# Kernel tuning notes

Hardware: AMD Instinct MI355X
Metric: run time of the kernel (lower is better)

Reference implementation:

```python
import jax, jax.numpy as jnp
import numpy as np

S, V, E, H = 4096, 10000, 128, 256
NE, TK, NH, HD, FF, NL = 4, 2, 4, 64, 2048, 2
EPS = 1e-5
SCALE = 1.0 / np.sqrt(HD).astype(np.float32)


def setup_inputs() -> dict:
    key = jax.random.key(0)
    ks = iter(jax.random.split(key, 64))
    n = lambda shape: jax.random.normal(next(ks), shape, jnp.float32) * 0.02
    inp = {"x": jax.random.randint(next(ks), (S,), 0, V)}
    inp["emb"] = n((V, E))
    for i, din in enumerate([E, H, H]):
        inp[f"moe{i}_gw"] = n((NE, din))
        inp[f"moe{i}_gb"] = jnp.zeros((NE,), jnp.float32)
        inp[f"moe{i}_ew"] = n((NE, H, din))
        inp[f"moe{i}_eb"] = jnp.zeros((NE, H), jnp.float32)
    inp["attn_in_w"] = n((NL, 3 * H, H)); inp["attn_in_b"] = jnp.zeros((NL, 3 * H), jnp.float32)
    inp["attn_out_w"] = n((NL, H, H));    inp["attn_out_b"] = jnp.zeros((NL, H), jnp.float32)
    inp["ln1_g"] = jnp.ones((NL, H), jnp.float32); inp["ln1_b"] = jnp.zeros((NL, H), jnp.float32)
    inp["ln2_g"] = jnp.ones((NL, H), jnp.float32); inp["ln2_b"] = jnp.zeros((NL, H), jnp.float32)
    inp["ff1_w"] = n((NL, FF, H)); inp["ff1_b"] = jnp.zeros((NL, FF), jnp.float32)
    inp["ff2_w"] = n((NL, H, FF)); inp["ff2_b"] = jnp.zeros((NL, H), jnp.float32)
    inp["fc_w"] = n((H, H)); inp["fc_b"] = jnp.zeros((H,), jnp.float32)
    inp["out_w"] = n((V, H)); inp["out_b"] = jnp.zeros((V,), jnp.float32)
    return inp


def _ln(x, g, b):
    m = x.mean(-1, keepdims=True)
    v = ((x - m) ** 2).mean(-1, keepdims=True)
    return (x - m) * jax.lax.rsqrt(v + EPS) * g + b


def _moe(x, gw, gb, ew, eb):
    # x: [S, din]. Faithful quirk: experts are the top-k of TOKEN 0's gates,
    # applied to every token, weighted by each token's own top-k gate scores.
    scores = jax.nn.softmax(x @ gw.T + gb, axis=-1)            # [S, NE]
    vals, idx = jax.lax.top_k(scores, TK)                      # [S, TK]
    sel = idx[0]                                               # [TK]
    outs = jnp.einsum('si,khi->skh', x, ew[sel]) + eb[sel][None]  # [S, TK, H]
    return (outs * vals[:, :, None]).sum(axis=1)               # [S, H]


def reference(x, emb,
              moe0_gw, moe0_gb, moe0_ew, moe0_eb,
              moe1_gw, moe1_gb, moe1_ew, moe1_eb,
              moe2_gw, moe2_gb, moe2_ew, moe2_eb,
              attn_in_w, attn_in_b, attn_out_w, attn_out_b,
              ln1_g, ln1_b, ln2_g, ln2_b,
              ff1_w, ff1_b, ff2_w, ff2_b,
              fc_w, fc_b, out_w, out_b):
    h = emb[x]                                                 # [S, E]
    for gw, gb, ew, eb in [(moe0_gw, moe0_gb, moe0_ew, moe0_eb),
                           (moe1_gw, moe1_gb, moe1_ew, moe1_eb),
                           (moe2_gw, moe2_gb, moe2_ew, moe2_eb)]:
        h = _moe(h, gw, gb, ew, eb)                            # [S, H]
    for l in range(NL):  # post-norm TransformerEncoderLayer (relu, no dropout at eval)
        qkv = h @ attn_in_w[l].T + attn_in_b[l]                # [S, 3H]
        q, k, v = [t.reshape(S, NH, HD) for t in jnp.split(qkv, 3, axis=-1)]
        att = jax.nn.softmax(jnp.einsum('shd,thd->hst', q, k) * SCALE, axis=-1)
        a = jnp.einsum('hst,thd->shd', att, v).reshape(S, H)
        h = _ln(h + a @ attn_out_w[l].T + attn_out_b[l], ln1_g[l], ln1_b[l])
        ffh = jax.nn.relu(h @ ff1_w[l].T + ff1_b[l]) @ ff2_w[l].T + ff2_b[l]
        h = _ln(h + ffh, ln2_g[l], ln2_b[l])
    h = h @ fc_w.T + fc_b                                      # [S, H]
    logits = h @ out_w.T + out_b                               # [S, V]
    return jax.nn.log_softmax(logits, axis=-1)
```

## Files before the change

kernel.cpp:

```cpp
#include <hip/hip_runtime.h>
#include <math.h>

#define S_ 4096
#define V_ 10000
#define E_ 128
#define H_ 256
#define NE_ 4
#define NH_ 4
#define HD_ 64
#define FF_ 2048
#define NL_ 2
#define EPS_ 1e-5f
#define SCALE_ 0.125f
#define SPLITS_ 4
#define PSTRIDE_ 160

typedef __attribute__((ext_vector_type(8))) short bf16x8;
typedef __attribute__((ext_vector_type(4))) float f32x4;

static __device__ __forceinline__ short f2bf(float f) {
  unsigned u = __builtin_bit_cast(unsigned, f);
  unsigned r = (u + 0x7fffu + ((u >> 16) & 1u)) >> 16;
  return (short)r;
}
static __device__ __forceinline__ float bf2f(short s) {
  unsigned u = ((unsigned)(unsigned short)s) << 16;
  return __builtin_bit_cast(float, u);
}

struct CvtArgs {
  const float* src[9];
  short* dst[9];
  int pfx[10];
};
__global__ __launch_bounds__(256) void k_cvt(CvtArgs a, const int* __restrict__ x,
                                             const float* __restrict__ emb,
                                             short* __restrict__ h) {
  int b = blockIdx.x;
  if (b >= a.pfx[9]) {
    int i8 = (b - a.pfx[9]) * 2048 + threadIdx.x * 8;
    int s = i8 >> 7, e = i8 & 127;
    const float* sp = &emb[(size_t)x[s] * E_ + e];
    float4 v0 = *(const float4*)sp;
    float4 v1 = *(const float4*)(sp + 4);
    short4 o0, o1;
    o0.x = f2bf(v0.x); o0.y = f2bf(v0.y); o0.z = f2bf(v0.z); o0.w = f2bf(v0.w);
    o1.x = f2bf(v1.x); o1.y = f2bf(v1.y); o1.z = f2bf(v1.z); o1.w = f2bf(v1.w);
    *(short4*)&h[i8] = o0;
    *(short4*)&h[i8 + 4] = o1;
    return;
  }
  int s = 0;
  while (b >= a.pfx[s + 1]) ++s;
  size_t base = (size_t)(b - a.pfx[s]) * 2048 + threadIdx.x * 8;
  const float* sp = a.src[s] + base;
  short* dp = a.dst[s] + base;
  float4 v0 = *(const float4*)sp;
  float4 v1 = *(const float4*)(sp + 4);
  short4 o0, o1;
  o0.x = f2bf(v0.x); o0.y = f2bf(v0.y); o0.z = f2bf(v0.z); o0.w = f2bf(v0.w);
  o1.x = f2bf(v1.x); o1.y = f2bf(v1.y); o1.z = f2bf(v1.z); o1.w = f2bf(v1.w);
  *(short4*)dp = o0;
  *(short4*)(dp + 4) = o1;
}

__global__ __launch_bounds__(256) void k_gates(const short* __restrict__ X, int din,
                                               const float* __restrict__ gw,
                                               const float* __restrict__ gb,
                                               float* __restrict__ vals,
                                               int* __restrict__ sel) {
  int wave = threadIdx.x >> 6, lane = threadIdx.x & 63;
  int s = blockIdx.x * 4 + wave;
  const short* xs = X + (size_t)s * din;
  float a0 = 0.f, a1 = 0.f, a2 = 0.f, a3 = 0.f;
  for (int i = lane; i < din; i += 64) {
    float xv = bf2f(xs[i]);
    a0 += xv * gw[0 * din + i];
    a1 += xv * gw[1 * din + i];
    a2 += xv * gw[2 * din + i];
    a3 += xv * gw[3 * din + i];
  }
#pragma unroll
  for (int off = 32; off > 0; off >>= 1) {
    a0 += __shfl_xor(a0, off, 64);
    a1 += __shfl_xor(a1, off, 64);
    a2 += __shfl_xor(a2, off, 64);
    a3 += __shfl_xor(a3, off, 64);
  }
  if (lane == 0) {
    float sc[4] = {a0 + gb[0], a1 + gb[1], a2 + gb[2], a3 + gb[3]};
    float mx = fmaxf(fmaxf(sc[0], sc[1]), fmaxf(sc[2], sc[3]));
    float sum = 0.f;
#pragma unroll
    for (int e = 0; e < 4; ++e) { sc[e] = expf(sc[e] - mx); sum += sc[e]; }
    float inv = 1.0f / sum;
#pragma unroll
    for (int e = 0; e < 4; ++e) sc[e] *= inv;
    int i0 = 0; float v0 = sc[0];
#pragma unroll
    for (int e = 1; e < 4; ++e) if (sc[e] > v0) { v0 = sc[e]; i0 = e; }
    float v1 = -1.0f; int i1 = 0;
#pragma unroll
    for (int e = 0; e < 4; ++e) if (e != i0 && sc[e] > v1) { v1 = sc[e]; i1 = e; }
    vals[2 * s + 0] = v0;
    vals[2 * s + 1] = v1;
    if (s == 0) { sel[0] = i0; sel[1] = i1; }
  }
}

template <int ACT>
__global__ __launch_bounds__(256) void k_gemm64(const short* __restrict__ A,
                                                const short* __restrict__ W,
                                                const float* __restrict__ bias,
                                                short* __restrict__ C,
                                                int M, int N, int K) {
  __shared__ short As[64][40];
  __shared__ short Bs[64][40];
  int bm = blockIdx.y * 64, bn = blockIdx.x * 64;
  int tid = threadIdx.x, lane = tid & 63, wv = tid >> 6;
  int quad = lane >> 4, m16 = lane & 15;
  int wr = (wv >> 1) * 32, wc = (wv & 1) * 32;
  int srow = tid >> 2, sc = (tid & 3) * 8;
  const short* Ar = A + (size_t)(bm + srow) * K + sc;
  const short* Wr = W + (size_t)(bn + srow) * K + sc;
  f32x4 acc[2][2];
#pragma unroll
  for (int m = 0; m < 2; ++m)
#pragma unroll
    for (int n = 0; n < 2; ++n) acc[m][n] = (f32x4){0.f, 0.f, 0.f, 0.f};
  for (int k0 = 0; k0 < K; k0 += 32) {
    *(bf16x8*)&As[srow][sc] = *(const bf16x8*)&Ar[k0];
    *(bf16x8*)&Bs[srow][sc] = *(const bf16x8*)&Wr[k0];
    __syncthreads();
    bf16x8 af[2], bf[2];
#pragma unroll
    for (int m = 0; m < 2; ++m) af[m] = *(const bf16x8*)&As[wr + m * 16 + m16][quad * 8];
#pragma unroll
    for (int n = 0; n < 2; ++n) bf[n] = *(const bf16x8*)&Bs[wc + n * 16 + m16][quad * 8];
#pragma unroll
    for (int m = 0; m < 2; ++m)
#pragma unroll
      for (int n = 0; n < 2; ++n)
        acc[m][n] = __builtin_amdgcn_mfma_f32_16x16x32_bf16(af[m], bf[n], acc[m][n], 0, 0, 0);
    __syncthreads();
  }
#pragma unroll
  for (int n = 0; n < 2; ++n) {
    int col = bn + wc + n * 16 + m16;
    float b = bias[col];
#pragma unroll
    for (int m = 0; m < 2; ++m) {
      int row0 = bm + wr + m * 16 + quad * 4;
#pragma unroll
      for (int r = 0; r < 4; ++r) {
        float v = acc[m][n][r] + b;
        if (ACT) v = fmaxf(v, 0.f);
        C[(size_t)(row0 + r) * N + col] = f2bf(v);
      }
    }
  }
}

template <int ACT>
__global__ __launch_bounds__(256) void k_gemm32(const short* __restrict__ A,
                                                const short* __restrict__ W,
                                                const float* __restrict__ bias,
                                                short* __restrict__ C,
                                                int M, int N, int K) {
  __shared__ short As[32][40];
  __shared__ short Bs[64][40];
  int bm = blockIdx.y * 32, bn = blockIdx.x * 64;
  int tid = threadIdx.x, lane = tid & 63, wv = tid >> 6;
  int quad = lane >> 4, m16 = lane & 15;
  int wr = (wv >> 1) * 16, wc = (wv & 1) * 32;
  int srow = tid >> 2, sc = (tid & 3) * 8;
  const short* Ar = A + (size_t)(bm + (srow & 31)) * K + sc;
  const short* Wr = W + (size_t)(bn + srow) * K + sc;
  f32x4 acc[2];
  acc[0] = (f32x4){0.f, 0.f, 0.f, 0.f};
  acc[1] = (f32x4){0.f, 0.f, 0.f, 0.f};
  for (int k0 = 0; k0 < K; k0 += 32) {
    if (tid < 128) *(bf16x8*)&As[srow][sc] = *(const bf16x8*)&Ar[k0];
    *(bf16x8*)&Bs[srow][sc] = *(const bf16x8*)&Wr[k0];
    __syncthreads();
    bf16x8 af = *(const bf16x8*)&As[wr + m16][quad * 8];
    bf16x8 bf0 = *(const bf16x8*)&Bs[wc + m16][quad * 8];
    bf16x8 bf1 = *(const bf16x8*)&Bs[wc + 16 + m16][quad * 8];
    acc[0] = __builtin_amdgcn_mfma_f32_16x16x32_bf16(af, bf0, acc[0], 0, 0, 0);
    acc[1] = __builtin_amdgcn_mfma_f32_16x16x32_bf16(af, bf1, acc[1], 0, 0, 0);
    __syncthreads();
  }
#pragma unroll
  for (int n = 0; n < 2; ++n) {
    int col = bn + wc + n * 16 + m16;
    float b = bias[col];
    int row0 = bm + wr + quad * 4;
#pragma unroll
    for (int r = 0; r < 4; ++r) {
      float v = acc[n][r] + b;
      if (ACT) v = fmaxf(v, 0.f);
      C[(size_t)(row0 + r) * N + col] = f2bf(v);
    }
  }
}

__global__ __launch_bounds__(256) void k_proj(const float* __restrict__ Opart,
                                              const float* __restrict__ Lpart,
                                              const short* __restrict__ W,
                                              const float* __restrict__ bias,
                                              short* __restrict__ C) {
  __shared__ short As[32][40];
  __shared__ short Bs[64][40];
  int bm = blockIdx.y * 32, bn = blockIdx.x * 64;
  int tid = threadIdx.x, lane = tid & 63, wv = tid >> 6;
  int quad = lane >> 4, m16 = lane & 15;
  int wr = (wv >> 1) * 16, wc = (wv & 1) * 32;
  int srow = tid >> 2, sc = (tid & 3) * 8;
  int rowA = bm + (srow & 31);
  const short* Wr = W + (size_t)(bn + srow) * H_ + sc;
  float invden[NH_];
  if (tid < 128) {
#pragma unroll
    for (int hh = 0; hh < NH_; ++hh) {
      float dsum = 0.f;
#pragma unroll
      for (int sp = 0; sp < SPLITS_; ++sp)
        dsum += Lpart[(size_t)(sp * NH_ + hh) * S_ + rowA];
      invden[hh] = 1.0f / dsum;
    }
  }
  f32x4 acc[2];
  acc[0] = (f32x4){0.f, 0.f, 0.f, 0.f};
  acc[1] = (f32x4){0.f, 0.f, 0.f, 0.f};
#pragma unroll
  for (int k0 = 0; k0 < H_; k0 += 32) {
    if (tid < 128) {
      const int head = k0 >> 6;
      int dd = (k0 & 63) + sc;
      float n0 = 0.f, n1 = 0.f, n2 = 0.f, n3 = 0.f, n4 = 0.f, n5 = 0.f, n6 = 0.f, n7 = 0.f;
#pragma unroll
      for (int sp = 0; sp < SPLITS_; ++sp) {
        const float* op = &Opart[((size_t)(sp * NH_ + head) * S_ + rowA) * 64 + dd];
        float4 u0 = *(const float4*)op;
        float4 u1 = *(const float4*)(op + 4);
        n0 += u0.x; n1 += u0.y; n2 += u0.z; n3 += u0.w;
        n4 += u1.x; n5 += u1.y; n6 += u1.z; n7 += u1.w;
      }
      float iv = invden[head];
      union { short s[8]; bf16x8 v; } o;
      o.s[0] = f2bf(n0 * iv); o.s[1] = f2bf(n1 * iv);
      o.s[2] = f2bf(n2 * iv); o.s[3] = f2bf(n3 * iv);
      o.s[4] = f2bf(n4 * iv); o.s[5] = f2bf(n5 * iv);
      o.s[6] = f2bf(n6 * iv); o.s[7] = f2bf(n7 * iv);
      *(bf16x8*)&As[srow][sc] = o.v;
    }
    *(bf16x8*)&Bs[srow][sc] = *(const bf16x8*)&Wr[k0];
    __syncthreads();
    bf16x8 af = *(const bf16x8*)&As[wr + m16][quad * 8];
    bf16x8 bf0 = *(const bf16x8*)&Bs[wc + m16][quad * 8];
    bf16x8 bf1 = *(const bf16x8*)&Bs[wc + 16 + m16][quad * 8];
    acc[0] = __builtin_amdgcn_mfma_f32_16x16x32_bf16(af, bf0, acc[0], 0, 0, 0);
    acc[1] = __builtin_amdgcn_mfma_f32_16x16x32_bf16(af, bf1, acc[1], 0, 0, 0);
    __syncthreads();
  }
#pragma unroll
  for (int n = 0; n < 2; ++n) {
    int col = bn + wc + n * 16 + m16;
    float b = bias[col];
    int row0 = bm + wr + quad * 4;
#pragma unroll
    for (int r = 0; r < 4; ++r) {
      float v = acc[n][r] + b;
      C[(size_t)(row0 + r) * H_ + col] = f2bf(v);
    }
  }
}

__global__ __launch_bounds__(256) void k_ff2(const short* __restrict__ A,
                                             const short* __restrict__ W,
                                             const float* __restrict__ bias,
                                             short* __restrict__ C) {
  __shared__ short As[32][72];
  __shared__ short Bs[64][72];
  int bm = blockIdx.y * 32, bn = blockIdx.x * 64;
  int tid = threadIdx.x, lane = tid & 63, wv = tid >> 6;
  int quad = lane >> 4, m16 = lane & 15;
  int wr = (wv >> 1) * 16, wc = (wv & 1) * 32;
  int arow = tid >> 3, ac = (tid & 7) * 8;
  int brow = tid >> 2, bc = (tid & 3) * 16;
  const short* Ar = A + (size_t)(bm + arow) * FF_ + ac;
  const short* Wr = W + (size_t)(bn + brow) * FF_ + bc;
  f32x4 acc[2];
  acc[0] = (f32x4){0.f, 0.f, 0.f, 0.f};
  acc[1] = (f32x4){0.f, 0.f, 0.f, 0.f};
  for (int k0 = 0; k0 < FF_; k0 += 64) {
    *(bf16x8*)&As[arow][ac] = *(const bf16x8*)&Ar[k0];
    *(bf16x8*)&Bs[brow][bc] = *(const bf16x8*)&Wr[k0];
    *(bf16x8*)&Bs[brow][bc + 8] = *(const bf16x8*)&Wr[k0 + 8];
    __syncthreads();
    bf16x8 af0 = *(const bf16x8*)&As[wr + m16][quad * 8];
    bf16x8 af1 = *(const bf16x8*)&As[wr + m16][32 + quad * 8];
    bf16x8 b00 = *(const bf16x8*)&Bs[wc + m16][quad * 8];
    bf16x8 b01 = *(const bf16x8*)&Bs[wc + m16][32 + quad * 8];
    bf16x8 b10 = *(const bf16x8*)&Bs[wc + 16 + m16][quad * 8];
    bf16x8 b11 = *(const bf16x8*)&Bs[wc + 16 + m16][32 + quad * 8];
    acc[0] = __builtin_amdgcn_mfma_f32_16x16x32_bf16(af0, b00, acc[0], 0, 0, 0);
    acc[0] = __builtin_amdgcn_mfma_f32_16x16x32_bf16(af1, b01, acc[0], 0, 0, 0);
    acc[1] = __builtin_amdgcn_mfma_f32_16x16x32_bf16(af0, b10, acc[1], 0, 0, 0);
    acc[1] = __builtin_amdgcn_mfma_f32_16x16x32_bf16(af1, b11, acc[1], 0, 0, 0);
    __syncthreads();
  }
#pragma unroll
  for (int n = 0; n < 2; ++n) {
    int col = bn + wc + n * 16 + m16;
    float b = bias[col];
    int row0 = bm + wr + quad * 4;
#pragma unroll
    for (int r = 0; r < 4; ++r) {
      float v = acc[n][r] + b;
      C[(size_t)(row0 + r) * H_ + col] = f2bf(v);
    }
  }
}

__global__ __launch_bounds__(256) void k_moe(const short* __restrict__ A,
                                             const short* __restrict__ EW,
                                             const float* __restrict__ EB,
                                             const float* __restrict__ vals,
                                             const int* __restrict__ sel,
                                             short* __restrict__ C,
                                             int N, int K) {
  __shared__ short As[32][40];
  __shared__ short B0s[64][40];
  __shared__ short B1s[64][40];
  int e0 = sel[0], e1 = sel[1];
  const short* W0 = EW + (size_t)e0 * N * K;
  const short* W1 = EW + (size_t)e1 * N * K;
  const float* b0 = EB + (size_t)e0 * N;
  const float* b1 = EB + (size_t)e1 * N;
  int bm = blockIdx.y * 32, bn = blockIdx.x * 64;
  int tid = threadIdx.x, lane = tid & 63, wv = tid >> 6;
  int quad = lane >> 4, m16 = lane & 15;
  int wr = (wv >> 1) * 16, wc = (wv & 1) * 32;
  int srow = tid >> 2, sc = (tid & 3) * 8;
  const short* Ar = A + (size_t)(bm + (srow & 31)) * K + sc;
  const short* W0r = W0 + (size_t)(bn + srow) * K + sc;
  const short* W1r = W1 + (size_t)(bn + srow) * K + sc;
  f32x4 a0[2], a1[2];
  a0[0] = a0[1] = (f32x4){0.f, 0.f, 0.f, 0.f};
  a1[0] = a1[1] = (f32x4){0.f, 0.f, 0.f, 0.f};
  for (int k0 = 0; k0 < K; k0 += 32) {
    if (tid < 128) *(bf16x8*)&As[srow][sc] = *(const bf16x8*)&Ar[k0];
    *(bf16x8*)&B0s[srow][sc] = *(const bf16x8*)&W0r[k0];
    *(bf16x8*)&B1s[srow][sc] = *(const bf16x8*)&W1r[k0];
    __syncthreads();
    bf16x8 af = *(const bf16x8*)&As[wr + m16][quad * 8];
#pragma unroll
    for (int n = 0; n < 2; ++n) {
      bf16x8 bf0 = *(const bf16x8*)&B0s[wc + n * 16 + m16][quad * 8];
      bf16x8 bf1 = *(const bf16x8*)&B1s[wc + n * 16 + m16][quad * 8];
      a0[n] = __builtin_amdgcn_mfma_f32_16x16x32_bf16(af, bf0, a0[n], 0, 0, 0);
      a1[n] = __builtin_amdgcn_mfma_f32_16x16x32_bf16(af, bf1, a1[n], 0, 0, 0);
    }
    __syncthreads();
  }
#pragma unroll
  for (int n = 0; n < 2; ++n) {
    int col = bn + wc + n * 16 + m16;
    float bb0 = b0[col], bb1 = b1[col];
    int row0 = bm + wr + quad * 4;
#pragma unroll
    for (int r = 0; r < 4; ++r) {
      int row = row0 + r;
      float v = vals[2 * row] * (a0[n][r] + bb0) + vals[2 * row + 1] * (a1[n][r] + bb1);
      C[(size_t)row * N + col] = f2bf(v);
    }
  }
}

template <int ACT>
__global__ __launch_bounds__(256) void k_gemm128(const short* __restrict__ A,
                                                 const short* __restrict__ W,
                                                 const float* __restrict__ bias,
                                                 short* __restrict__ C,
                                                 int M, int N, int K) {
  __shared__ short As[128][40];
  __shared__ short Bs[128][40];
  int bm = blockIdx.y * 128, bn = blockIdx.x * 128;
  int tid = threadIdx.x, lane = tid & 63, wv = tid >> 6;
  int quad = lane >> 4, m16 = lane & 15;
  int wr = (wv >> 1) * 64, wc = (wv & 1) * 64;
  int srow = tid >> 1, sc = (tid & 1) * 16;
  const short* Ar = A + (size_t)(bm + srow) * K + sc;
  const short* Wr = W + (size_t)(bn + srow) * K + sc;
  f32x4 acc[4][4];
#pragma unroll
  for (int m = 0; m < 4; ++m)
#pragma unroll
    for (int n = 0; n < 4; ++n) acc[m][n] = (f32x4){0.f, 0.f, 0.f, 0.f};
  for (int k0 = 0; k0 < K; k0 += 32) {
    *(bf16x8*)&As[srow][sc] = *(const bf16x8*)&Ar[k0];
    *(bf16x8*)&As[srow][sc + 8] = *(const bf16x8*)&Ar[k0 + 8];
    *(bf16x8*)&Bs[srow][sc] = *(const bf16x8*)&Wr[k0];
    *(bf16x8*)&Bs[srow][sc + 8] = *(const bf16x8*)&Wr[k0 + 8];
    __syncthreads();
    bf16x8 af[4], bf[4];
#pragma unroll
    for (int m = 0; m < 4; ++m) af[m] = *(const bf16x8*)&As[wr + m * 16 + m16][quad * 8];
#pragma unroll
    for (int n = 0; n < 4; ++n) bf[n] = *(const bf16x8*)&Bs[wc + n * 16 + m16][quad * 8];
#pragma unroll
    for (int m = 0; m < 4; ++m)
#pragma unroll
      for (int n = 0; n < 4; ++n)
        acc[m][n] = __builtin_amdgcn_mfma_f32_16x16x32_bf16(af[m], bf[n], acc[m][n], 0, 0, 0);
    __syncthreads();
  }
#pragma unroll
  for (int n = 0; n < 4; ++n) {
    int col = bn + wc + n * 16 + m16;
    float b = bias[col];
#pragma unroll
    for (int m = 0; m < 4; ++m) {
      int row0 = bm + wr + m * 16 + quad * 4;
#pragma unroll
      for (int r = 0; r < 4; ++r) {
        float v = acc[m][n][r] + b;
        if (ACT) v = fmaxf(v, 0.f);
        C[(size_t)(row0 + r) * N + col] = f2bf(v);
      }
    }
  }
}

__global__ __launch_bounds__(256) void k_gsum(const short* __restrict__ A,
                                              const short* __restrict__ W,
                                              const float* __restrict__ bias,
                                              float* __restrict__ psums,
                                              int M, int N, int K) {
  __shared__ short As[128][40];
  __shared__ short Bs[128][40];
  int bm = blockIdx.y * 128, bn = blockIdx.x * 128;
  int tid = threadIdx.x, lane = tid & 63, wv = tid >> 6;
  int quad = lane >> 4, m16 = lane & 15;
  int wr = (wv >> 1) * 64, wc = (wv & 1) * 64;
  int srow = tid >> 1, sc = (tid & 1) * 16;
  const short* Ar = A + (size_t)(bm + srow) * K + sc;
  int br = bn + srow;
  const short* Wr = W + (size_t)(br < N ? br : N - 1) * K + sc;
  f32x4 acc[4][4];
#pragma unroll
  for (int m = 0; m < 4; ++m)
#pragma unroll
    for (int n = 0; n < 4; ++n) acc[m][n] = (f32x4){0.f, 0.f, 0.f, 0.f};
  for (int k0 = 0; k0 < K; k0 += 32) {
    *(bf16x8*)&As[srow][sc] = *(const bf16x8*)&Ar[k0];
    *(bf16x8*)&As[srow][sc + 8] = *(const bf16x8*)&Ar[k0 + 8];
    *(bf16x8*)&Bs[srow][sc] = *(const bf16x8*)&Wr[k0];
    *(bf16x8*)&Bs[srow][sc + 8] = *(const bf16x8*)&Wr[k0 + 8];
    __syncthreads();
    bf16x8 af[4], bf[4];
#pragma unroll
    for (int m = 0; m < 4; ++m) af[m] = *(const bf16x8*)&As[wr + m * 16 + m16][quad * 8];
#pragma unroll
    for (int n = 0; n < 4; ++n) bf[n] = *(const bf16x8*)&Bs[wc + n * 16 + m16][quad * 8];
#pragma unroll
    for (int m = 0; m < 4; ++m)
#pragma unroll
      for (int n = 0; n < 4; ++n)
        acc[m][n] = __builtin_amdgcn_mfma_f32_16x16x32_bf16(af[m], bf[n], acc[m][n], 0, 0, 0);
    __syncthreads();
  }
  float bcol[4];
  int cvalid[4];
#pragma unroll
  for (int n = 0; n < 4; ++n) {
    int col = bn + wc + n * 16 + m16;
    cvalid[n] = (col < N);
    bcol[n] = cvalid[n] ? bias[col] : 0.f;
  }
  int pslot = blockIdx.x * 2 + (wv & 1);
#pragma unroll
  for (int m = 0; m < 4; ++m) {
#pragma unroll
    for (int r = 0; r < 4; ++r) {
      int row = bm + wr + m * 16 + quad * 4 + r;
      float es = 0.f;
#pragma unroll
      for (int n = 0; n < 4; ++n) {
        if (cvalid[n]) {
          float v = acc[m][n][r] + bcol[n];
          es += __expf(v);
        }
      }
#pragma unroll
      for (int mask = 1; mask < 16; mask <<= 1) es += __shfl_xor(es, mask, 16);
      if (m16 == 0) psums[(size_t)row * PSTRIDE_ + pslot] = es;
    }
  }
}

__global__ __launch_bounds__(256) void k_lse(const float* __restrict__ psums,
                                             float* __restrict__ lse, int nslots) {
  int wv = threadIdx.x >> 6, lane = threadIdx.x & 63;
  int s = blockIdx.x * 4 + wv;
  float a = 0.f;
  for (int i = lane; i < nslots; i += 64) a += psums[(size_t)s * PSTRIDE_ + i];
#pragma unroll
  for (int mask = 1; mask < 64; mask <<= 1) a += __shfl_xor(a, mask, 64);
  if (lane == 0) lse[s] = logf(a);
}

__global__ __launch_bounds__(256) void k_gout(const short* __restrict__ A,
                                              const short* __restrict__ W,
                                              const float* __restrict__ bias,
                                              const float* __restrict__ lse,
                                              float* __restrict__ C,
                                              int M, int N, int K) {
  __shared__ short As[128][40];
  __shared__ short Bs[128][40];
  int bm = blockIdx.y * 128, bn = blockIdx.x * 128;
  int tid = threadIdx.x, lane = tid & 63, wv = tid >> 6;
  int quad = lane >> 4, m16 = lane & 15;
  int wr = (wv >> 1) * 64, wc = (wv & 1) * 64;
  int srow = tid >> 1, sc = (tid & 1) * 16;
  const short* Ar = A + (size_t)(bm + srow) * K + sc;
  int br = bn + srow;
  const short* Wr = W + (size_t)(br < N ? br : N - 1) * K + sc;
  f32x4 acc[4][4];
#pragma unroll
  for (int m = 0; m < 4; ++m)
#pragma unroll
    for (int n = 0; n < 4; ++n) acc[m][n] = (f32x4){0.f, 0.f, 0.f, 0.f};
  for (int k0 = 0; k0 < K; k0 += 32) {
    *(bf16x8*)&As[srow][sc] = *(const bf16x8*)&Ar[k0];
    *(bf16x8*)&As[srow][sc + 8] = *(const bf16x8*)&Ar[k0 + 8];
    *(bf16x8*)&Bs[srow][sc] = *(const bf16x8*)&Wr[k0];
    *(bf16x8*)&Bs[srow][sc + 8] = *(const bf16x8*)&Wr[k0 + 8];
    __syncthreads();
    bf16x8 af[4], bf[4];
#pragma unroll
    for (int m = 0; m < 4; ++m) af[m] = *(const bf16x8*)&As[wr + m * 16 + m16][quad * 8];
#pragma unroll
    for (int n = 0; n < 4; ++n) bf[n] = *(const bf16x8*)&Bs[wc + n * 16 + m16][quad * 8];
#pragma unroll
    for (int m = 0; m < 4; ++m)
#pragma unroll
      for (int n = 0; n < 4; ++n)
        acc[m][n] = __builtin_amdgcn_mfma_f32_16x16x32_bf16(af[m], bf[n], acc[m][n], 0, 0, 0);
    __syncthreads();
  }
  float bcol[4];
  int cvalid[4];
#pragma unroll
  for (int n = 0; n < 4; ++n) {
    int col = bn + wc + n * 16 + m16;
    cvalid[n] = (col < N);
    bcol[n] = cvalid[n] ? bias[col] : 0.f;
  }
#pragma unroll
  for (int m = 0; m < 4; ++m) {
#pragma unroll
    for (int r = 0; r < 4; ++r) {
      int row = bm + wr + m * 16 + quad * 4 + r;
      float flse = lse[row];
#pragma unroll
      for (int n = 0; n < 4; ++n) {
        if (cvalid[n]) {
          float v = acc[m][n][r] + bcol[n] - flse;
          C[(size_t)row * N + (bn + wc + n * 16 + m16)] = v;
        }
      }
    }
  }
}

__global__ __launch_bounds__(256) void k_attn(const short* __restrict__ qkv,
                                              float* __restrict__ Opart,
                                              float* __restrict__ Lpart) {
  __shared__ short Ks[64][72];
  __shared__ short Vt[64][72];
  int tid = threadIdx.x, lane = tid & 63, wv = tid >> 6;
  int quad = lane >> 4, m16 = lane & 15;
  int head = blockIdx.y, hd0 = head * HD_;
  int split = blockIdx.z;
  int qbaseA = blockIdx.x * 128 + wv * 16;
  int qbaseB = qbaseA + 64;
  bf16x8 qfA[2], qfB[2];
  {
    const short* qrA = qkv + (size_t)(qbaseA + m16) * (3 * H_) + hd0 + quad * 8;
    qfA[0] = *(const bf16x8*)&qrA[0];
    qfA[1] = *(const bf16x8*)&qrA[32];
    const short* qrB = qkv + (size_t)(qbaseB + m16) * (3 * H_) + hd0 + quad * 8;
    qfB[0] = *(const bf16x8*)&qrB[0];
    qfB[1] = *(const bf16x8*)&qrB[32];
  }
  f32x4 oA[4], oB[4];
#pragma unroll
  for (int dt = 0; dt < 4; ++dt) {
    oA[dt] = (f32x4){0.f, 0.f, 0.f, 0.f};
    oB[dt] = (f32x4){0.f, 0.f, 0.f, 0.f};
  }
  float lA = 0.f, lB = 0.f;

  int kb_end = (split + 1) * (S_ / 64 / SPLITS_);
  for (int kb = split * (S_ / 64 / SPLITS_); kb < kb_end; ++kb) {
    __syncthreads();
    {
      int key = tid >> 2, d0 = (tid & 3) * 16;
      const short* kr = qkv + (size_t)(kb * 64 + key) * (3 * H_) + H_ + hd0 + d0;
      *(bf16x8*)&Ks[key][d0] = *(const bf16x8*)&kr[0];
      *(bf16x8*)&Ks[key][d0 + 8] = *(const bf16x8*)&kr[8];
    }
    {
      int key0 = (tid & 15) * 4, d0 = (tid >> 4) * 4;
      const short* vbase = qkv + (size_t)(kb * 64 + key0) * (3 * H_) + 2 * H_ + hd0 + d0;
      short4 v0 = *(const short4*)&vbase[0];
      short4 v1 = *(const short4*)&vbase[3 * H_];
// ... 128 lines not shown
  for (int i = 0; i < 4; ++i) { d[i] = x[i] - mean; vs += d[i] * d[i]; }
#pragma unroll
  for (int mask = 1; mask < 64; mask <<= 1) vs += __shfl_xor(vs, mask, 64);
  float inv = rsqrtf(vs * (1.0f / H_) + EPS_);
  float4 gv = *(const float4*)&g[lane * 4];
  float4 bv = *(const float4*)&b[lane * 4];
  short4 ov;
  ov.x = f2bf(d[0] * inv * gv.x + bv.x);
  ov.y = f2bf(d[1] * inv * gv.y + bv.y);
  ov.z = f2bf(d[2] * inv * gv.z + bv.z);
  ov.w = f2bf(d[3] * inv * gv.w + bv.w);
  *(short4*)&h[off] = ov;
}

extern "C" void kernel_launch(void* const* d_in, const int* in_sizes, int n_in,
                              void* d_out, int out_size, void* d_ws, size_t ws_size,
                              hipStream_t stream) {
  const int* x = (const int*)d_in[0];
  const float* emb = (const float*)d_in[1];
  const float* moe_gw[3] = {(const float*)d_in[2], (const float*)d_in[6], (const float*)d_in[10]};
  const float* moe_gb[3] = {(const float*)d_in[3], (const float*)d_in[7], (const float*)d_in[11]};
  const float* moe_eb[3] = {(const float*)d_in[5], (const float*)d_in[9], (const float*)d_in[13]};
  const float* attn_in_b = (const float*)d_in[15];
  const float* attn_out_b = (const float*)d_in[17];
  const float* ln1_g = (const float*)d_in[18];
  const float* ln1_b = (const float*)d_in[19];
  const float* ln2_g = (const float*)d_in[20];
  const float* ln2_b = (const float*)d_in[21];
  const float* ff1_b = (const float*)d_in[23];
  const float* ff2_b = (const float*)d_in[25];
  const float* fc_b = (const float*)d_in[27];
  const float* out_b = (const float*)d_in[29];
  float* out = (float*)d_out;

  short* wsS = (short*)d_ws;
  size_t off = 0;
  auto alloc = [&](size_t n) { short* p = wsS + off; off += n; return p; };
  short* ewb0 = alloc(131072);
  short* ewb1 = alloc(262144);
  short* ewb2 = alloc(262144);
  short* aiwb = alloc(393216);
  short* aowb = alloc(131072);
  short* f1wb = alloc(1048576);
  short* f2wb = alloc(1048576);
  short* fcwb = alloc(65536);
  short* owb  = alloc(2560000);
  short* hb_e = alloc((size_t)S_ * E_);
  short* hb_a = alloc((size_t)S_ * H_);
  short* hb_b = alloc((size_t)S_ * H_);
  short* qkvb = alloc((size_t)S_ * 3 * H_);
  short* abufb = alloc((size_t)S_ * H_);
  short* tmpb = alloc((size_t)S_ * H_);
  short* ffhb = alloc((size_t)S_ * FF_);
  float* vals = (float*)(wsS + off); off += 2 * (size_t)S_ * 2;
  int* sel = (int*)(wsS + off);
  float* Opart = (float*)ffhb;
  float* Lpart = (float*)tmpb;
  float* psums = (float*)f1wb;
  float* lse = psums + (size_t)S_ * PSTRIDE_;

  const short* moe_ewb[3] = {ewb0, ewb1, ewb2};

  CvtArgs ca;
  ca.src[0] = (const float*)d_in[4];  ca.dst[0] = ewb0;
  ca.src[1] = (const float*)d_in[8];  ca.dst[1] = ewb1;
  ca.src[2] = (const float*)d_in[12]; ca.dst[2] = ewb2;
  ca.src[3] = (const float*)d_in[14]; ca.dst[3] = aiwb;
  ca.src[4] = (const float*)d_in[16]; ca.dst[4] = aowb;
  ca.src[5] = (const float*)d_in[22]; ca.dst[5] = f1wb;
  ca.src[6] = (const float*)d_in[24]; ca.dst[6] = f2wb;
  ca.src[7] = (const float*)d_in[26]; ca.dst[7] = fcwb;
  ca.src[8] = (const float*)d_in[28]; ca.dst[8] = owb;
  int sizes[9] = {131072, 262144, 262144, 393216, 131072, 1048576, 1048576, 65536, 2560000};
  ca.pfx[0] = 0;
  for (int i = 0; i < 9; ++i) ca.pfx[i + 1] = ca.pfx[i] + sizes[i] / 2048;
  k_cvt<<<dim3(ca.pfx[9] + S_ * E_ / 2048), dim3(256), 0, stream>>>(ca, x, emb, hb_e);

  const short* moe_in[3] = {hb_e, hb_a, hb_b};
  short* moe_out[3] = {hb_a, hb_b, hb_a};
  int moe_k[3] = {E_, H_, H_};
  for (int i = 0; i < 3; ++i) {
    k_gates<<<dim3(S_ / 4), dim3(256), 0, stream>>>(moe_in[i], moe_k[i], moe_gw[i], moe_gb[i], vals, sel);
    k_moe<<<dim3(H_ / 64, S_ / 32), dim3(256), 0, stream>>>(moe_in[i], moe_ewb[i], moe_eb[i],
                                                            vals, sel, moe_out[i], H_, moe_k[i]);
  }

  for (int l = 0; l < NL_; ++l) {
    k_gemm64<0><<<dim3(3 * H_ / 64, S_ / 64), dim3(256), 0, stream>>>(
        hb_a, aiwb + (size_t)l * 3 * H_ * H_, attn_in_b + (size_t)l * 3 * H_, qkvb, S_, 3 * H_, H_);
    k_attn<<<dim3(S_ / 128, NH_, SPLITS_), dim3(256), 0, stream>>>(qkvb, Opart, Lpart);
    k_proj<<<dim3(H_ / 64, S_ / 32), dim3(256), 0, stream>>>(
        Opart, Lpart, aowb + (size_t)l * H_ * H_, attn_out_b + (size_t)l * H_, tmpb);
    k_add_ln<<<dim3(S_ / 4), dim3(256), 0, stream>>>(hb_a, tmpb, ln1_g + l * H_, ln1_b + l * H_);
    k_gemm128<1><<<dim3(FF_ / 128, S_ / 128), dim3(256), 0, stream>>>(
        hb_a, f1wb + (size_t)l * FF_ * H_, ff1_b + (size_t)l * FF_, ffhb, S_, FF_, H_);
    k_ff2<<<dim3(H_ / 64, S_ / 32), dim3(256), 0, stream>>>(
        ffhb, f2wb + (size_t)l * H_ * FF_, ff2_b + (size_t)l * H_, tmpb);
    k_add_ln<<<dim3(S_ / 4), dim3(256), 0, stream>>>(hb_a, tmpb, ln2_g + l * H_, ln2_b + l * H_);
  }

  k_gemm32<0><<<dim3(H_ / 64, S_ / 32), dim3(256), 0, stream>>>(hb_a, fcwb, fc_b, tmpb, S_, H_, H_);
  int nxb = (V_ + 127) / 128;
  k_gsum<<<dim3(nxb, S_ / 128), dim3(256), 0, stream>>>(tmpb, owb, out_b, psums, S_, V_, H_);
  k_lse<<<dim3(S_ / 4), dim3(256), 0, stream>>>(psums, lse, nxb * 2);
  k_gout<<<dim3(nxb, S_ / 128), dim3(256), 0, stream>>>(tmpb, owb, out_b, lse, out, S_, V_, H_);
}
```

Measured before the change: 582.6 us.

## Fuse MoE gating and LSE reduction into consumers, widen GEMM K-tiles to 64

Gate scoring, softmax and top-k now run inside the MoE GEMM kernel, with each block recomputing token 0's gates for expert selection. The separate log-sum-exp kernel is folded into the output kernel's prologue. The 64- and 128-tile GEMMs now stage 64-wide K slices per barrier instead of 32, and the fc layer reuses the ff2 kernel. The aim is fewer launches and fewer barriers per K step, at the cost of redundant gate and LSE work per block and more LDS per block.

```diff
diff --git a/kernel.cpp b/kernel.cpp
--- a/kernel.cpp
+++ b/kernel.cpp
@@ -64,84 +64,45 @@
   *(short4*)(dp + 4) = o1;
 }
 
-__global__ __launch_bounds__(256) void k_gates(const short* __restrict__ X, int din,
-                                               const float* __restrict__ gw,
-                                               const float* __restrict__ gb,
-                                               float* __restrict__ vals,
-                                               int* __restrict__ sel) {
-  int wave = threadIdx.x >> 6, lane = threadIdx.x & 63;
-  int s = blockIdx.x * 4 + wave;
-  const short* xs = X + (size_t)s * din;
-  float a0 = 0.f, a1 = 0.f, a2 = 0.f, a3 = 0.f;
-  for (int i = lane; i < din; i += 64) {
-    float xv = bf2f(xs[i]);
-    a0 += xv * gw[0 * din + i];
-    a1 += xv * gw[1 * din + i];
-    a2 += xv * gw[2 * din + i];
-    a3 += xv * gw[3 * din + i];
-  }
-#pragma unroll
-  for (int off = 32; off > 0; off >>= 1) {
-    a0 += __shfl_xor(a0, off, 64);
-    a1 += __shfl_xor(a1, off, 64);
-    a2 += __shfl_xor(a2, off, 64);
-    a3 += __shfl_xor(a3, off, 64);
-  }
-  if (lane == 0) {
-    float sc[4] = {a0 + gb[0], a1 + gb[1], a2 + gb[2], a3 + gb[3]};
-    float mx = fmaxf(fmaxf(sc[0], sc[1]), fmaxf(sc[2], sc[3]));
-    float sum = 0.f;
-#pragma unroll
-    for (int e = 0; e < 4; ++e) { sc[e] = expf(sc[e] - mx); sum += sc[e]; }
-    float inv = 1.0f / sum;
-#pragma unroll
-    for (int e = 0; e < 4; ++e) sc[e] *= inv;
-    int i0 = 0; float v0 = sc[0];
-#pragma unroll
-    for (int e = 1; e < 4; ++e) if (sc[e] > v0) { v0 = sc[e]; i0 = e; }
-    float v1 = -1.0f; int i1 = 0;
-#pragma unroll
-    for (int e = 0; e < 4; ++e) if (e != i0 && sc[e] > v1) { v1 = sc[e]; i1 = e; }
-    vals[2 * s + 0] = v0;
-    vals[2 * s + 1] = v1;
-    if (s == 0) { sel[0] = i0; sel[1] = i1; }
-  }
-}
-
 template <int ACT>
 __global__ __launch_bounds__(256) void k_gemm64(const short* __restrict__ A,
                                                 const short* __restrict__ W,
                                                 const float* __restrict__ bias,
                                                 short* __restrict__ C,
                                                 int M, int N, int K) {
-  __shared__ short As[64][40];
-  __shared__ short Bs[64][40];
+  __shared__ short As[64][72];
+  __shared__ short Bs[64][72];
   int bm = blockIdx.y * 64, bn = blockIdx.x * 64;
   int tid = threadIdx.x, lane = tid & 63, wv = tid >> 6;
   int quad = lane >> 4, m16 = lane & 15;
   int wr = (wv >> 1) * 32, wc = (wv & 1) * 32;
-  int srow = tid >> 2, sc = (tid & 3) * 8;
-  const short* Ar = A + (size_t)(bm + srow) * K + sc;
-  const short* Wr = W + (size_t)(bn + srow) * K + sc;
+  int srow = tid >> 2, scc = (tid & 3) * 16;
+  const short* Ar = A + (size_t)(bm + srow) * K + scc;
+  const short* Wr = W + (size_t)(bn + srow) * K + scc;
   f32x4 acc[2][2];
 #pragma unroll
   for (int m = 0; m < 2; ++m)
 #pragma unroll
     for (int n = 0; n < 2; ++n) acc[m][n] = (f32x4){0.f, 0.f, 0.f, 0.f};
-  for (int k0 = 0; k0 < K; k0 += 32) {
-    *(bf16x8*)&As[srow][sc] = *(const bf16x8*)&Ar[k0];
-    *(bf16x8*)&Bs[srow][sc] = *(const bf16x8*)&Wr[k0];
-    __syncthreads();
-    bf16x8 af[2], bf[2];
-#pragma unroll
-    for (int m = 0; m < 2; ++m) af[m] = *(const bf16x8*)&As[wr + m * 16 + m16][quad * 8];
-#pragma unroll
-    for (int n = 0; n < 2; ++n) bf[n] = *(const bf16x8*)&Bs[wc + n * 16 + m16][quad * 8];
-#pragma unroll
-    for (int m = 0; m < 2; ++m)
-#pragma unroll
-      for (int n = 0; n < 2; ++n)
-        acc[m][n] = __builtin_amdgcn_mfma_f32_16x16x32_bf16(af[m], bf[n], acc[m][n], 0, 0, 0);
+  for (int k0 = 0; k0 < K; k0 += 64) {
+    *(bf16x8*)&As[srow][scc] = *(const bf16x8*)&Ar[k0];
+    *(bf16x8*)&As[srow][scc + 8] = *(const bf16x8*)&Ar[k0 + 8];
+    *(bf16x8*)&Bs[srow][scc] = *(const bf16x8*)&Wr[k0];
+    *(bf16x8*)&Bs[srow][scc + 8] = *(const bf16x8*)&Wr[k0 + 8];
+    __syncthreads();
+#pragma unroll
+    for (int kk = 0; kk < 2; ++kk) {
+      bf16x8 af[2], bf[2];
+#pragma unroll
+      for (int m = 0; m < 2; ++m) af[m] = *(const bf16x8*)&As[wr + m * 16 + m16][kk * 32 + quad * 8];
+#pragma unroll
+      for (int n = 0; n < 2; ++n) bf[n] = *(const bf16x8*)&Bs[wc + n * 16 + m16][kk * 32 + quad * 8];
+#pragma unroll
+      for (int m = 0; m < 2; ++m)
+#pragma unroll
+        for (int n = 0; n < 2; ++n)
+          acc[m][n] = __builtin_amdgcn_mfma_f32_16x16x32_bf16(af[m], bf[n], acc[m][n], 0, 0, 0);
+    }
     __syncthreads();
   }
 #pragma unroll
@@ -157,49 +118,6 @@
         if (ACT) v = fmaxf(v, 0.f);
         C[(size_t)(row0 + r) * N + col] = f2bf(v);
       }
-    }
-  }
-}
-
-template <int ACT>
-__global__ __launch_bounds__(256) void k_gemm32(const short* __restrict__ A,
-                                                const short* __restrict__ W,
-                                                const float* __restrict__ bias,
-                                                short* __restrict__ C,
-                                                int M, int N, int K) {
-  __shared__ short As[32][40];
-  __shared__ short Bs[64][40];
-  int bm = blockIdx.y * 32, bn = blockIdx.x * 64;
-  int tid = threadIdx.x, lane = tid & 63, wv = tid >> 6;
-  int quad = lane >> 4, m16 = lane & 15;
-  int wr = (wv >> 1) * 16, wc = (wv & 1) * 32;
-  int srow = tid >> 2, sc = (tid & 3) * 8;
-  const short* Ar = A + (size_t)(bm + (srow & 31)) * K + sc;
-  const short* Wr = W + (size_t)(bn + srow) * K + sc;
-  f32x4 acc[2];
-  acc[0] = (f32x4){0.f, 0.f, 0.f, 0.f};
-  acc[1] = (f32x4){0.f, 0.f, 0.f, 0.f};
-  for (int k0 = 0; k0 < K; k0 += 32) {
-    if (tid < 128) *(bf16x8*)&As[srow][sc] = *(const bf16x8*)&Ar[k0];
-    *(bf16x8*)&Bs[srow][sc] = *(const bf16x8*)&Wr[k0];
-    __syncthreads();
-    bf16x8 af = *(const bf16x8*)&As[wr + m16][quad * 8];
-    bf16x8 bf0 = *(const bf16x8*)&Bs[wc + m16][quad * 8];
-    bf16x8 bf1 = *(const bf16x8*)&Bs[wc + 16 + m16][quad * 8];
-    acc[0] = __builtin_amdgcn_mfma_f32_16x16x32_bf16(af, bf0, acc[0], 0, 0, 0);
-    acc[1] = __builtin_amdgcn_mfma_f32_16x16x32_bf16(af, bf1, acc[1], 0, 0, 0);
-    __syncthreads();
-  }
-#pragma unroll
-  for (int n = 0; n < 2; ++n) {
-    int col = bn + wc + n * 16 + m16;
-    float b = bias[col];
-    int row0 = bm + wr + quad * 4;
-#pragma unroll
-    for (int r = 0; r < 4; ++r) {
-      float v = acc[n][r] + b;
-      if (ACT) v = fmaxf(v, 0.f);
-      C[(size_t)(row0 + r) * N + col] = f2bf(v);
     }
   }
 }
@@ -279,7 +197,7 @@
 __global__ __launch_bounds__(256) void k_ff2(const short* __restrict__ A,
                                              const short* __restrict__ W,
                                              const float* __restrict__ bias,
-                                             short* __restrict__ C) {
+                                             short* __restrict__ C, int K) {
   __shared__ short As[32][72];
   __shared__ short Bs[64][72];
   int bm = blockIdx.y * 32, bn = blockIdx.x * 64;
@@ -288,12 +206,12 @@
   int wr = (wv >> 1) * 16, wc = (wv & 1) * 32;
   int arow = tid >> 3, ac = (tid & 7) * 8;
   int brow = tid >> 2, bc = (tid & 3) * 16;
-  const short* Ar = A + (size_t)(bm + arow) * FF_ + ac;
-  const short* Wr = W + (size_t)(bn + brow) * FF_ + bc;
+  const short* Ar = A + (size_t)(bm + arow) * K + ac;
+  const short* Wr = W + (size_t)(bn + brow) * K + bc;
   f32x4 acc[2];
   acc[0] = (f32x4){0.f, 0.f, 0.f, 0.f};
   acc[1] = (f32x4){0.f, 0.f, 0.f, 0.f};
-  for (int k0 = 0; k0 < FF_; k0 += 64) {
+  for (int k0 = 0; k0 < K; k0 += 64) {
     *(bf16x8*)&As[arow][ac] = *(const bf16x8*)&Ar[k0];
     *(bf16x8*)&Bs[brow][bc] = *(const bf16x8*)&Wr[k0];
     *(bf16x8*)&Bs[brow][bc + 8] = *(const bf16x8*)&Wr[k0 + 8];
@@ -326,26 +244,95 @@
 __global__ __launch_bounds__(256) void k_moe(const short* __restrict__ A,
                                              const short* __restrict__ EW,
                                              const float* __restrict__ EB,
-                                             const float* __restrict__ vals,
-                                             const int* __restrict__ sel,
+                                             const float* __restrict__ gw,
+                                             const float* __restrict__ gb,
                                              short* __restrict__ C,
                                              int N, int K) {
   __shared__ short As[32][40];
   __shared__ short B0s[64][40];
   __shared__ short B1s[64][40];
-  int e0 = sel[0], e1 = sel[1];
-  const short* W0 = EW + (size_t)e0 * N * K;
-  const short* W1 = EW + (size_t)e1 * N * K;
-  const float* b0 = EB + (size_t)e0 * N;
-  const float* b1 = EB + (size_t)e1 * N;
+  __shared__ float sc_lds[32][NE_];
+  __shared__ float g0_lds[NE_];
+  __shared__ float vals_lds[32][2];
+  __shared__ int sel_lds[2];
   int bm = blockIdx.y * 32, bn = blockIdx.x * 64;
   int tid = threadIdx.x, lane = tid & 63, wv = tid >> 6;
   int quad = lane >> 4, m16 = lane & 15;
   int wr = (wv >> 1) * 16, wc = (wv & 1) * 32;
   int srow = tid >> 2, sc = (tid & 3) * 8;
+  if (tid < 128) {
+    int r = tid & 31, e = tid >> 5;
+    const short* xs = A + (size_t)(bm + r) * K;
+    const float* w = gw + (size_t)e * K;
+    float acc = 0.f;
+    for (int i = 0; i < K; i += 8) {
+      bf16x8 xv = *(const bf16x8*)&xs[i];
+      float4 w0 = *(const float4*)&w[i];
+      float4 w1 = *(const float4*)&w[i + 4];
+      acc += bf2f(xv[0]) * w0.x + bf2f(xv[1]) * w0.y + bf2f(xv[2]) * w0.z + bf2f(xv[3]) * w0.w;
+      acc += bf2f(xv[4]) * w1.x + bf2f(xv[5]) * w1.y + bf2f(xv[6]) * w1.z + bf2f(xv[7]) * w1.w;
+    }
+    sc_lds[r][e] = acc + gb[e];
+  } else if (tid < 132) {
+    int e = tid - 128;
+    const float* w = gw + (size_t)e * K;
+    float acc = 0.f;
+    for (int i = 0; i < K; i += 8) {
+      bf16x8 xv = *(const bf16x8*)&A[i];
+      float4 w0 = *(const float4*)&w[i];
+      float4 w1 = *(const float4*)&w[i + 4];
+      acc += bf2f(xv[0]) * w0.x + bf2f(xv[1]) * w0.y + bf2f(xv[2]) * w0.z + bf2f(xv[3]) * w0.w;
+      acc += bf2f(xv[4]) * w1.x + bf2f(xv[5]) * w1.y + bf2f(xv[6]) * w1.z + bf2f(xv[7]) * w1.w;
+    }
+    g0_lds[e] = acc + gb[e];
+  }
+  __syncthreads();
+  if (tid < 32) {
+    float g[4];
+#pragma unroll
+    for (int e = 0; e < 4; ++e) g[e] = sc_lds[tid][e];
+    float mx = fmaxf(fmaxf(g[0], g[1]), fmaxf(g[2], g[3]));
+    float sum = 0.f;
+#pragma unroll
+    for (int e = 0; e < 4; ++e) { g[e] = __expf(g[e] - mx); sum += g[e]; }
+    float inv = 1.0f / sum;
+#pragma unroll
+    for (int e = 0; e < 4; ++e) g[e] *= inv;
+    int i0 = 0; float v0 = g[0];
+#pragma unroll
+    for (int e = 1; e < 4; ++e) if (g[e] > v0) { v0 = g[e]; i0 = e; }
+    float v1 = -1.0f;
+#pragma unroll
+    for (int e = 0; e < 4; ++e) if (e != i0 && g[e] > v1) v1 = g[e];
+    vals_lds[tid][0] = v0;
+    vals_lds[tid][1] = v1;
+  } else if (tid == 32) {
+    float g[4];
+#pragma unroll
+    for (int e = 0; e < 4; ++e) g[e] = g0_lds[e];
+    float mx = fmaxf(fmaxf(g[0], g[1]), fmaxf(g[2], g[3]));
+    float sum = 0.f;
+#pragma unroll
+    for (int e = 0; e < 4; ++e) { g[e] = __expf(g[e] - mx); sum += g[e]; }
+    float inv = 1.0f / sum;
+#pragma unroll
+    for (int e = 0; e < 4; ++e) g[e] *= inv;
+    int i0 = 0; float v0 = g[0];
+#pragma unroll
+    for (int e = 1; e < 4; ++e) if (g[e] > v0) { v0 = g[e]; i0 = e; }
+    int i1 = 0; float v1 = -1.0f;
+#pragma unroll
+    for (int e = 0; e < 4; ++e) if (e != i0 && g[e] > v1) { v1 = g[e]; i1 = e; }
+    sel_lds[0] = i0;
+    sel_lds[1] = i1;
+  }
+  __syncthreads();
+  int e0 = sel_lds[0], e1 = sel_lds[1];
+  const short* W0r = EW + (size_t)e0 * N * K + (size_t)(bn + srow) * K + sc;
+  const short* W1r = EW + (size_t)e1 * N * K + (size_t)(bn + srow) * K + sc;
+  const float* b0 = EB + (size_t)e0 * N;
+  const float* b1 = EB + (size_t)e1 * N;
   const short* Ar = A + (size_t)(bm + (srow & 31)) * K + sc;
-  const short* W0r = W0 + (size_t)(bn + srow) * K + sc;
-  const short* W1r = W1 + (size_t)(bn + srow) * K + sc;
   f32x4 a0[2], a1[2];
   a0[0] = a0[1] = (f32x4){0.f, 0.f, 0.f, 0.f};
   a1[0] = a1[1] = (f32x4){0.f, 0.f, 0.f, 0.f};
@@ -368,12 +355,12 @@
   for (int n = 0; n < 2; ++n) {
     int col = bn + wc + n * 16 + m16;
     float bb0 = b0[col], bb1 = b1[col];
-    int row0 = bm + wr + quad * 4;
+    int row0 = wr + quad * 4;
 #pragma unroll
     for (int r = 0; r < 4; ++r) {
-      int row = row0 + r;
-      float v = vals[2 * row] * (a0[n][r] + bb0) + vals[2 * row + 1] * (a1[n][r] + bb1);
-      C[(size_t)row * N + col] = f2bf(v);
+      int lrow = row0 + r;
+      float v = vals_lds[lrow][0] * (a0[n][r] + bb0) + vals_lds[lrow][1] * (a1[n][r] + bb1);
+      C[(size_t)(bm + lrow) * N + col] = f2bf(v);
     }
   }
 }
@@ -438,13 +425,13 @@
                                               const float* __restrict__ bias,
                                               float* __restrict__ psums,
                                               int M, int N, int K) {
-  __shared__ short As[128][40];
-  __shared__ short Bs[128][40];
+  __shared__ short As[128][72];
+  __shared__ short Bs[128][72];
   int bm = blockIdx.y * 128, bn = blockIdx.x * 128;
   int tid = threadIdx.x, lane = tid & 63, wv = tid >> 6;
   int quad = lane >> 4, m16 = lane & 15;
   int wr = (wv >> 1) * 64, wc = (wv & 1) * 64;
-  int srow = tid >> 1, sc = (tid & 1) * 16;
+  int srow = tid >> 1, sc = (tid & 1) * 32;
   const short* Ar = A + (size_t)(bm + srow) * K + sc;
   int br = bn + srow;
   const short* Wr = W + (size_t)(br < N ? br : N - 1) * K + sc;
@@ -453,22 +440,29 @@
   for (int m = 0; m < 4; ++m)
 #pragma unroll
     for (int n = 0; n < 4; ++n) acc[m][n] = (f32x4){0.f, 0.f, 0.f, 0.f};
-  for (int k0 = 0; k0 < K; k0 += 32) {
+  for (int k0 = 0; k0 < K; k0 += 64) {
     *(bf16x8*)&As[srow][sc] = *(const bf16x8*)&Ar[k0];
     *(bf16x8*)&As[srow][sc + 8] = *(const bf16x8*)&Ar[k0 + 8];
+    *(bf16x8*)&As[srow][sc + 16] = *(const bf16x8*)&Ar[k0 + 16];
+    *(bf16x8*)&As[srow][sc + 24] = *(const bf16x8*)&Ar[k0 + 24];
     *(bf16x8*)&Bs[srow][sc] = *(const bf16x8*)&Wr[k0];
     *(bf16x8*)&Bs[srow][sc + 8] = *(const bf16x8*)&Wr[k0 + 8];
-    __syncthreads();
-    bf16x8 af[4], bf[4];
-#pragma unroll
-    for (int m = 0; m < 4; ++m) af[m] = *(const bf16x8*)&As[wr + m * 16 + m16][quad * 8];
-#pragma unroll
-    for (int n = 0; n < 4; ++n) bf[n] = *(const bf16x8*)&Bs[wc + n * 16 + m16][quad * 8];
-#pragma unroll
-    for (int m = 0; m < 4; ++m)
-#pragma unroll
-      for (int n = 0; n < 4; ++n)
-        acc[m][n] = __builtin_amdgcn_mfma_f32_16x16x32_bf16(af[m], bf[n], acc[m][n], 0, 0, 0);
+    *(bf16x8*)&Bs[srow][sc + 16] = *(const bf16x8*)&Wr[k0 + 16];
+    *(bf16x8*)&Bs[srow][sc + 24] = *(const bf16x8*)&Wr[k0 + 24];
+    __syncthreads();
+#pragma unroll
+    for (int kk = 0; kk < 2; ++kk) {
+      bf16x8 af[4], bf[4];
+#pragma unroll
+      for (int m = 0; m < 4; ++m) af[m] = *(const bf16x8*)&As[wr + m * 16 + m16][kk * 32 + quad * 8];
+#pragma unroll
+      for (int n = 0; n < 4; ++n) bf[n] = *(const bf16x8*)&Bs[wc + n * 16 + m16][kk * 32 + quad * 8];
+#pragma unroll
+      for (int m = 0; m < 4; ++m)
+#pragma unroll
+        for (int n = 0; n < 4; ++n)
+          acc[m][n] = __builtin_amdgcn_mfma_f32_16x16x32_bf16(af[m], bf[n], acc[m][n], 0, 0, 0);
+    }
     __syncthreads();
   }
   float bcol[4];
@@ -500,30 +494,26 @@
   }
 }
 
-__global__ __launch_bounds__(256) void k_lse(const float* __restrict__ psums,
-                                             float* __restrict__ lse, int nslots) {
-  int wv = threadIdx.x >> 6, lane = threadIdx.x & 63;
-  int s = blockIdx.x * 4 + wv;
-  float a = 0.f;
-  for (int i = lane; i < nslots; i += 64) a += psums[(size_t)s * PSTRIDE_ + i];
-#pragma unroll
-  for (int mask = 1; mask < 64; mask <<= 1) a += __shfl_xor(a, mask, 64);
-  if (lane == 0) lse[s] = logf(a);
-}
-
 __global__ __launch_bounds__(256) void k_gout(const short* __restrict__ A,
                                               const short* __restrict__ W,
                                               const float* __restrict__ bias,
-                                              const float* __restrict__ lse,
+                                              const float* __restrict__ psums,
                                               float* __restrict__ C,
-                                              int M, int N, int K) {
-  __shared__ short As[128][40];
-  __shared__ short Bs[128][40];
+                                              int M, int N, int K, int nslots) {
+  __shared__ short As[128][72];
+  __shared__ short Bs[128][72];
+  __shared__ float lse_lds[128];
   int bm = blockIdx.y * 128, bn = blockIdx.x * 128;
   int tid = threadIdx.x, lane = tid & 63, wv = tid >> 6;
   int quad = lane >> 4, m16 = lane & 15;
   int wr = (wv >> 1) * 64, wc = (wv & 1) * 64;
-  int srow = tid >> 1, sc = (tid & 1) * 16;
+  int srow = tid >> 1, sc = (tid & 1) * 32;
+  if (tid < 128) {
+    const float* pr = psums + (size_t)(bm + tid) * PSTRIDE_;
+    float a = 0.f;
+    for (int i = 0; i < nslots; ++i) a += pr[i];
+    lse_lds[tid] = logf(a);
+  }
   const short* Ar = A + (size_t)(bm + srow) * K + sc;
   int br = bn + srow;
   const short* Wr = W + (size_t)(br < N ? br : N - 1) * K + sc;
@@ -532,22 +522,29 @@
   for (int m = 0; m < 4; ++m)
 #pragma unroll
     for (int n = 0; n < 4; ++n) acc[m][n] = (f32x4){0.f, 0.f, 0.f, 0.f};
-  for (int k0 = 0; k0 < K; k0 += 32) {
+  for (int k0 = 0; k0 < K; k0 += 64) {
     *(bf16x8*)&As[srow][sc] = *(const bf16x8*)&Ar[k0];
     *(bf16x8*)&As[srow][sc + 8] = *(const bf16x8*)&Ar[k0 + 8];
+    *(bf16x8*)&As[srow][sc + 16] = *(const bf16x8*)&Ar[k0 + 16];
+    *(bf16x8*)&As[srow][sc + 24] = *(const bf16x8*)&Ar[k0 + 24];
     *(bf16x8*)&Bs[srow][sc] = *(const bf16x8*)&Wr[k0];
     *(bf16x8*)&Bs[srow][sc + 8] = *(const bf16x8*)&Wr[k0 + 8];
-    __syncthreads();
-    bf16x8 af[4], bf[4];
-#pragma unroll
-    for (int m = 0; m < 4; ++m) af[m] = *(const bf16x8*)&As[wr + m * 16 + m16][quad * 8];
-#pragma unroll
-    for (int n = 0; n < 4; ++n) bf[n] = *(const bf16x8*)&Bs[wc + n * 16 + m16][quad * 8];
-#pragma unroll
-    for (int m = 0; m < 4; ++m)
-#pragma unroll
-      for (int n = 0; n < 4; ++n)
-        acc[m][n] = __builtin_amdgcn_mfma_f32_16x16x32_bf16(af[m], bf[n], acc[m][n], 0, 0, 0);
+    *(bf16x8*)&Bs[srow][sc + 16] = *(const bf16x8*)&Wr[k0 + 16];
+    *(bf16x8*)&Bs[srow][sc + 24] = *(const bf16x8*)&Wr[k0 + 24];
+    __syncthreads();
+#pragma unroll
+    for (int kk = 0; kk < 2; ++kk) {
+      bf16x8 af[4], bf[4];
+#pragma unroll
+      for (int m = 0; m < 4; ++m) af[m] = *(const bf16x8*)&As[wr + m * 16 + m16][kk * 32 + quad * 8];
+#pragma unroll
+      for (int n = 0; n < 4; ++n) bf[n] = *(const bf16x8*)&Bs[wc + n * 16 + m16][kk * 32 + quad * 8];
+#pragma unroll
+      for (int m = 0; m < 4; ++m)
+#pragma unroll
+        for (int n = 0; n < 4; ++n)
+          acc[m][n] = __builtin_amdgcn_mfma_f32_16x16x32_bf16(af[m], bf[n], acc[m][n], 0, 0, 0);
+    }
     __syncthreads();
   }
   float bcol[4];
@@ -562,8 +559,9 @@
   for (int m = 0; m < 4; ++m) {
 #pragma unroll
     for (int r = 0; r < 4; ++r) {
-      int row = bm + wr + m * 16 + quad * 4 + r;
-      float flse = lse[row];
+      int lrow = wr + m * 16 + quad * 4 + r;
+      int row = bm + lrow;
+      float flse = lse_lds[lrow];
 #pragma unroll
       for (int n = 0; n < 4; ++n) {
         if (cvalid[n]) {
@@ -798,12 +796,9 @@
   short* abufb = alloc((size_t)S_ * H_);
   short* tmpb = alloc((size_t)S_ * H_);
   short* ffhb = alloc((size_t)S_ * FF_);
-  float* vals = (float*)(wsS + off); off += 2 * (size_t)S_ * 2;
-  int* sel = (int*)(wsS + off);
   float* Opart = (float*)ffhb;
   float* Lpart = (float*)tmpb;
   float* psums = (float*)f1wb;
-  float* lse = psums + (size_t)S_ * PSTRIDE_;
 
   const short* moe_ewb[3] = {ewb0, ewb1, ewb2};
 
@@ -826,9 +821,8 @@
   short* moe_out[3] = {hb_a, hb_b, hb_a};
   int moe_k[3] = {E_, H_, H_};
   for (int i = 0; i < 3; ++i) {
-    k_gates<<<dim3(S_ / 4), dim3(256), 0, stream>>>(moe_in[i], moe_k[i], moe_gw[i], moe_gb[i], vals, sel);
-    k_moe<<<dim3(H_ / 64, S_ / 32), dim3(256), 0, stream>>>(moe_in[i], moe_ewb[i], moe_eb[i],
-                                                            vals, sel, moe_out[i], H_, moe_k[i]);
+    k_moe<<<dim3(H_ / 64, S_ / 32), dim3(256), 0, stream>>>(
+        moe_in[i], moe_ewb[i], moe_eb[i], moe_gw[i], moe_gb[i], moe_out[i], H_, moe_k[i]);
   }
 
   for (int l = 0; l < NL_; ++l) {
@@ -841,13 +835,12 @@
     k_gemm128<1><<<dim3(FF_ / 128, S_ / 128), dim3(256), 0, stream>>>(
         hb_a, f1wb + (size_t)l * FF_ * H_, ff1_b + (size_t)l * FF_, ffhb, S_, FF_, H_);
     k_ff2<<<dim3(H_ / 64, S_ / 32), dim3(256), 0, stream>>>(
-        ffhb, f2wb + (size_t)l * H_ * FF_, ff2_b + (size_t)l * H_, tmpb);
+        ffhb, f2wb + (size_t)l * H_ * FF_, ff2_b + (size_t)l * H_, tmpb, FF_);
     k_add_ln<<<dim3(S_ / 4), dim3(256), 0, stream>>>(hb_a, tmpb, ln2_g + l * H_, ln2_b + l * H_);
   }
 
-  k_gemm32<0><<<dim3(H_ / 64, S_ / 32), dim3(256), 0, stream>>>(hb_a, fcwb, fc_b, tmpb, S_, H_, H_);
+  k_ff2<<<dim3(H_ / 64, S_ / 32), dim3(256), 0, stream>>>(hb_a, fcwb, fc_b, tmpb, H_);
   int nxb = (V_ + 127) / 128;
   k_gsum<<<dim3(nxb, S_ / 128), dim3(256), 0, stream>>>(tmpb, owb, out_b, psums, S_, V_, H_);
-  k_lse<<<dim3(S_ / 4), dim3(256), 0, stream>>>(psums, lse, nxb * 2);
-  k_gout<<<dim3(nxb, S_ / 128), dim3(256), 0, stream>>>(tmpb, owb, out_b, lse, out, S_, V_, H_);
-}
+  k_gout<<<dim3(nxb, S_ / 128), dim3(256), 0, stream>>>(tmpb, owb, out_b, psums, out, S_, V_, H_, nxb * 2);
+}
```

Result: slower. 754.3 us (+29.5%).
